# Performance work log

Measured on AMD Instinct MI355X. Metric: run time of the kernel, lower is better.

Reference implementation:

```python
import jax, jax.numpy as jnp
import numpy as np

BN_EPS = 1e-5
D_SLICE = 3  # forward slices last (neighbor) dim to :3 (d=3 in original code)


def _conv_bn_relu(x, W, b, gamma, beta):
    # x: (B, Cin, N, K) ; W: (Cout, Cin) ; 1x1 Conv2d + eval-mode BatchNorm(mean=0, var=1) + ReLU
    y = jnp.einsum('oi,bink->bonk', W, x) + b[:, None, None]
    y = gamma[:, None, None] * (y / jnp.sqrt(1.0 + BN_EPS)) + beta[:, None, None]
    return jax.nn.relu(y)


def setup_inputs() -> dict:
    key = jax.random.key(0)
    ks = jax.random.split(key, 16)
    B, N, K, C = 4, 32768, 16, 64
    mlp = [128, 64, 64]
    cin = C + 4  # feature + relation (diff_xyz 3 + distance 1)
    inp = {
        'src_xyz': jax.random.normal(ks[0], (B, 3, N, K), dtype=jnp.float32),
        'tgt_xyz': jax.random.normal(ks[1], (B, 3, N), dtype=jnp.float32),
        'feature': jax.random.normal(ks[2], (B, C, N, K), dtype=jnp.float32),
    }
    c_prev = cin
    for i, c_out in enumerate(mlp):
        scale = 1.0 / np.sqrt(c_prev)
        inp[f'W{i+1}'] = jax.random.uniform(ks[3 + 4 * i], (c_out, c_prev), minval=-scale, maxval=scale, dtype=jnp.float32)
        inp[f'b{i+1}'] = jax.random.uniform(ks[4 + 4 * i], (c_out,), minval=-scale, maxval=scale, dtype=jnp.float32)
        inp[f'g{i+1}'] = jnp.ones((c_out,), dtype=jnp.float32)
        inp[f'be{i+1}'] = jnp.zeros((c_out,), dtype=jnp.float32)
        c_prev = c_out
    return inp


def reference(src_xyz, tgt_xyz, feature, W1, b1, g1, be1, W2, b2, g2, be2, W3, b3, g3, be3):
    # relation feature on first D_SLICE neighbors (faithful to feature[:,:,:,:d], d=3)
    diff_xyz = src_xyz[:, :, :, :D_SLICE] - tgt_xyz[:, :, :, None]        # (B,3,N,3)
    distance = jnp.sum(diff_xyz ** 2, axis=1, keepdims=True)             # (B,1,N,3)
    x = jnp.concatenate([feature[:, :, :, :D_SLICE], diff_xyz, distance], axis=1)  # (B,C+4,N,3)
    x = _conv_bn_relu(x, W1, b1, g1, be1)
    x = _conv_bn_relu(x, W2, b2, g2, be2)
    x = _conv_bn_relu(x, W3, b3, g3, be3)
    return jnp.sum(x, axis=3)  # reduction='sum' over neighbor dim -> (B,64,N)
```

## Files before the change

kernel.cpp:

```cpp
#include <hip/hip_runtime.h>
#include <math.h>

typedef __attribute__((ext_vector_type(8))) short short8;
typedef __attribute__((ext_vector_type(4))) short short4v;
typedef __attribute__((ext_vector_type(4))) float f32x4;
typedef __attribute__((ext_vector_type(16))) float f32x16;

constexpr int BLOCK = 512;
constexpr int B_ = 4, C_ = 64, N_ = 32768, K_ = 16;
constexpr int P_ = 32;
constexpr int NCOL = 96;
constexpr int NF32 = 36, NF16 = 8;
constexpr int BIAS_OFF = (NF32 + NF16) * 1024;

constexpr int H2STR = 776;

__device__ __forceinline__ void bf16split(float f, short &hi, short &lo) {
    unsigned u  = __builtin_bit_cast(unsigned, f);
    unsigned hb = (u + 0x7FFFu + ((u >> 16) & 1u)) & 0xFFFF0000u;
    float hf    = __builtin_bit_cast(float, hb);
    hi = (short)(hb >> 16);
    float lf    = f - hf;
    unsigned ul = __builtin_bit_cast(unsigned, lf);
    lo = (short)((ul + 0x7FFFu + ((ul >> 16) & 1u)) >> 16);
}

__device__ __forceinline__ f32x4 mm16(short8 a, short8 b, f32x4 c) {
    return __builtin_amdgcn_mfma_f32_16x16x32_bf16(a, b, c, 0, 0, 0);
}
__device__ __forceinline__ f32x16 mm32(short8 a, short8 b, f32x16 c) {
    return __builtin_amdgcn_mfma_f32_32x32x16_bf16(a, b, c, 0, 0, 0);
}

__global__ void prep_wfrags(const float* __restrict__ W1, const float* __restrict__ g1,
                            const float* __restrict__ b1, const float* __restrict__ be1,
                            const float* __restrict__ W2, const float* __restrict__ g2,
                            const float* __restrict__ b2, const float* __restrict__ be2,
                            const float* __restrict__ W3, const float* __restrict__ g3,
                            const float* __restrict__ b3, const float* __restrict__ be3,
                            unsigned short* __restrict__ wf)
{
    const int gid = blockIdx.x * 256 + threadIdx.x;
    const float RS = 1.0f / sqrtf(1.0f + 1e-5f);
    const int NT = (NF32 + NF16) * 64;
    if (gid < NT) {
        const int f = gid >> 6, l = gid & 63;
        const float *W, *g; int CI, co, kb;
        if (f < 20)      { W = W1; g = g1; CI = 68;
                           co = (f / 5) * 32 + (l & 31);        kb = (f % 5) * 16 + (l >> 5) * 8; }
        else if (f < 36) { W = W2; g = g2; CI = 128;
                           co = ((f - 20) / 8) * 32 + (l & 31); kb = ((f - 20) % 8) * 16 + (l >> 5) * 8; }
        else             { W = W3; g = g3; CI = 64;
                           co = ((f - 36) / 2) * 16 + (l & 15); kb = ((f - 36) % 2) * 32 + (l >> 4) * 8; }
        const float gs = g[co] * RS;
        short8 h8, l8;
#pragma unroll
        for (int j = 0; j < 8; ++j) {
            const int k = kb + j;
            const float w = (k < CI) ? W[(size_t)co * CI + k] * gs : 0.0f;
            short hi, lo; bf16split(w, hi, lo);
            h8[j] = hi; l8[j] = lo;
        }
        *reinterpret_cast<short8*>(wf + (size_t)f * 1024 + l * 8)       = h8;
        *reinterpret_cast<short8*>(wf + (size_t)f * 1024 + 512 + l * 8) = l8;
    } else if (gid < NT + 256) {
        const int c = gid - NT;
        float* fb = reinterpret_cast<float*>(wf + BIAS_OFF);
        if (c < 128)      fb[c] = b1[c] * (g1[c] * RS) + be1[c];
        else if (c < 192) { const int q = c - 128; fb[c] = b2[q] * (g2[q] * RS) + be2[q]; }
        else              { const int q = c - 192; fb[c] = b3[q] * (g3[q] * RS) + be3[q]; }
    }
}

__device__ __forceinline__ void ldfrag(const unsigned short* __restrict__ wf,
                                       int f, int l, short8 &h, short8 &lo) {
    h  = *reinterpret_cast<const short8*>(wf + (size_t)f * 1024 + l * 8);
    lo = *reinterpret_cast<const short8*>(wf + (size_t)f * 1024 + 512 + l * 8);
}

__global__ __launch_bounds__(BLOCK, 4)
void mvp_mfma(const float* __restrict__ src, const float* __restrict__ tgt,
              const float* __restrict__ feat,
              const unsigned short* __restrict__ wf,
              float* __restrict__ out)
{
    __shared__ __align__(16) unsigned short xh_hi[10*768], xh_lo[10*768];
    __shared__ __align__(16) unsigned short h1_hi[16*768], h1_lo[16*768];

    const int tid = threadIdx.x;
    const int w   = tid >> 6;
    const int l   = tid & 63;
    const int b   = blockIdx.x >> 10;
    const int n0  = (blockIdx.x & 1023) << 5;

    if (tid < 96) {
        const int o = (9*96 + tid) * 8;
        const short8 z = {0,0,0,0,0,0,0,0};
        *reinterpret_cast<short8*>(&xh_hi[o]) = z;
        *reinterpret_cast<short8*>(&xh_lo[o]) = z;
    } else if (tid < 192) {
        const int o = (8*96 + (tid - 96)) * 8 + 4;
        const short4v z = {0,0,0,0};
        *reinterpret_cast<short4v*>(&xh_hi[o]) = z;
        *reinterpret_cast<short4v*>(&xh_lo[o]) = z;
    }
#pragma unroll
    for (int it = 0; it < 4; ++it) {
        const int idx = tid + it * BLOCK;
        const int c = idx >> 5, p = idx & 31;
        const float4 f = *reinterpret_cast<const float4*>(
            feat + ((size_t)(b*C_ + c) * N_ + (n0 + p)) * K_);
        const float v[3] = {f.x, f.y, f.z};
#pragma unroll
        for (int k = 0; k < 3; ++k) {
            short hi, lo; bf16split(v[k], hi, lo);
            const int off = ((c >> 3)*96 + k*32 + p)*8 + (c & 7);
            xh_hi[off] = (unsigned short)hi; xh_lo[off] = (unsigned short)lo;
        }
    }
    if (tid < 96) {
        const int p = tid & 31, k = tid >> 5;
        const int n = n0 + p;
        float d[4];
        d[0] = src[((size_t)(b*3+0)*N_ + n)*K_ + k] - tgt[(size_t)(b*3+0)*N_ + n];
        d[1] = src[((size_t)(b*3+1)*N_ + n)*K_ + k] - tgt[(size_t)(b*3+1)*N_ + n];
        d[2] = src[((size_t)(b*3+2)*N_ + n)*K_ + k] - tgt[(size_t)(b*3+2)*N_ + n];
        d[3] = d[0]*d[0] + d[1]*d[1] + d[2]*d[2];
        const int base = (8*96 + k*32 + p)*8;
#pragma unroll
        for (int j = 0; j < 4; ++j) {
            short hi, lo; bf16split(d[j], hi, lo);
            xh_hi[base + j] = (unsigned short)hi;
            xh_lo[base + j] = (unsigned short)lo;
        }
    }
    __syncthreads();

    const int hi32 = l >> 5, c32 = l & 31;
    const int lq = l >> 4, lr = l & 15, rq = lq << 2;
    const float* fb = reinterpret_cast<const float*>(wf + BIAS_OFF);

    {
        const int npass = (w < 4) ? 2 : 1;
        for (int pass = 0; pass < npass; ++pass) {
            const int t = pass ? (8 + w) : w;
            const int m = t / 3, n = t % 3;
            short8 ah[5], al[5];
#pragma unroll
            for (int ks = 0; ks < 5; ++ks) ldfrag(wf, m*5 + ks, l, ah[ks], al[ks]);
            f32x16 acc;
#pragma unroll
            for (int j = 0; j < 16; ++j) acc[j] = 0.0f;
#pragma unroll
            for (int ks = 0; ks < 5; ++ks) {
                const int so = ((ks*2 + hi32)*96 + n*32 + c32)*8;
                const short8 bh = *reinterpret_cast<const short8*>(&xh_hi[so]);
                const short8 bl = *reinterpret_cast<const short8*>(&xh_lo[so]);
                acc = mm32(ah[ks], bh, acc);
                acc = mm32(al[ks], bh, acc);
                acc = mm32(ah[ks], bl, acc);
            }
#pragma unroll
            for (int g = 0; g < 4; ++g) {
                const int co0 = m*32 + 8*g + 4*hi32;
                const float4 bb = *reinterpret_cast<const float4*>(fb + co0);
                const float bbv[4] = {bb.x, bb.y, bb.z, bb.w};
                short4v h4, l4;
#pragma unroll
                for (int r = 0; r < 4; ++r) {
                    const float v = fmaxf(acc[g*4 + r] + bbv[r], 0.0f);
                    short hh, ll; bf16split(v, hh, ll);
                    h4[r] = hh; l4[r] = ll;
                }
                const int so = ((m*4 + g)*96 + n*32 + c32)*8 + 4*hi32;
                *reinterpret_cast<short4v*>(&h1_hi[so]) = h4;
                *reinterpret_cast<short4v*>(&h1_lo[so]) = l4;
            }
        }
    }
    __syncthreads();

    if (w < 6) {
        const int m = w / 3, n = w % 3;
        short8 ah[8], al[8];
#pragma unroll
        for (int ks = 0; ks < 8; ++ks) ldfrag(wf, 20 + m*8 + ks, l, ah[ks], al[ks]);
        f32x16 acc;
#pragma unroll
        for (int j = 0; j < 16; ++j) acc[j] = 0.0f;
#pragma unroll
        for (int ks = 0; ks < 8; ++ks) {
            const int so = ((ks*2 + hi32)*96 + n*32 + c32)*8;
            const short8 bh = *reinterpret_cast<const short8*>(&h1_hi[so]);
            const short8 bl = *reinterpret_cast<const short8*>(&h1_lo[so]);
            acc = mm32(ah[ks], bh, acc);
            acc = mm32(al[ks], bh, acc);
            acc = mm32(ah[ks], bl, acc);
        }
#pragma unroll
        for (int g = 0; g < 4; ++g) {
            const int co0 = m*32 + 8*g + 4*hi32;
            const float4 bb = *reinterpret_cast<const float4*>(fb + 128 + co0);
            const float bbv[4] = {bb.x, bb.y, bb.z, bb.w};
            short4v h4, l4;
#pragma unroll
            for (int r = 0; r < 4; ++r) {
                const float v = fmaxf(acc[g*4 + r] + bbv[r], 0.0f);
                short hh, ll; bf16split(v, hh, ll);
                h4[r] = hh; l4[r] = ll;
            }
            const int so = (m*4 + g)*H2STR + (n*32 + c32)*8 + 4*hi32;
            *reinterpret_cast<short4v*>(&xh_hi[so]) = h4;
            *reinterpret_cast<short4v*>(&xh_lo[so]) = l4;
        }
    }
    __syncthreads();

    {
        const int m = w >> 1, hh = w & 1;
        short8 ah[2], al[2];
#pragma unroll
        for (int ks = 0; ks < 2; ++ks) ldfrag(wf, 36 + m*2 + ks, l, ah[ks], al[ks]);
        f32x4 acc3[3] = {f32x4{0,0,0,0}, f32x4{0,0,0,0}, f32x4{0,0,0,0}};
#pragma unroll
        for (int ks = 0; ks < 2; ++ks) {
#pragma unroll
            for (int t = 0; t < 3; ++t) {
                const int so = (ks*4 + lq)*H2STR + (t*32 + hh*16 + lr)*8;
                const short8 bh = *reinterpret_cast<const short8*>(&xh_hi[so]);
                const short8 bl = *reinterpret_cast<const short8*>(&xh_lo[so]);
                acc3[t] = mm16(ah[ks], bh, acc3[t]);
                acc3[t] = mm16(al[ks], bh, acc3[t]);
                acc3[t] = mm16(ah[ks], bl, acc3[t]);
            }
        }
        const int co0 = m*16 + rq;
        const float4 bb = *reinterpret_cast<const float4*>(fb + 192 + co0);
        const float bbv[4] = {bb.x, bb.y, bb.z, bb.w};
#pragma unroll
        for (int r = 0; r < 4; ++r) {
            float s = 0.0f;
#pragma unroll
            for (int t = 0; t < 3; ++t) s += fmaxf(acc3[t][r] + bbv[r], 0.0f);
            out[(size_t)(b*64 + co0 + r) * N_ + n0 + hh*16 + lr] = s;
        }
    }
}

extern "C" void kernel_launch(void* const* d_in, const int* in_sizes, int n_in,
                              void* d_out, int out_size, void* d_ws, size_t ws_size,
                              hipStream_t stream) {
    const float* src  = (const float*)d_in[0];
    const float* tgt  = (const float*)d_in[1];
    const float* feat = (const float*)d_in[2];
    const float* W1 = (const float*)d_in[3];
    const float* b1 = (const float*)d_in[4];
    const float* g1 = (const float*)d_in[5];
    const float* be1= (const float*)d_in[6];
    const float* W2 = (const float*)d_in[7];
    const float* b2 = (const float*)d_in[8];
    const float* g2 = (const float*)d_in[9];
    const float* be2= (const float*)d_in[10];
    const float* W3 = (const float*)d_in[11];
    const float* b3 = (const float*)d_in[12];
    const float* g3 = (const float*)d_in[13];
    const float* be3= (const float*)d_in[14];
    float* out = (float*)d_out;
    unsigned short* wfrag = (unsigned short*)d_ws;

    prep_wfrags<<<12, 256, 0, stream>>>(W1, g1, b1, be1, W2, g2, b2, be2,
                                        W3, g3, b3, be3, wfrag);

    const int grid = B_ * (N_ / P_);
    mvp_mfma<<<grid, BLOCK, 0, stream>>>(src, tgt, feat, wfrag, out);
}
```

Measured before the change: 159.6 us.

## Use fp16 single activations with split fp16 weights for layers two and three

Layers two and three now store hidden activations as one fp16 value instead of a bf16 hi/lo pair, and use fp16 MFMA with the weight split into fp16 hi plus residual. That drops one MFMA per step and halves LDS traffic for those activations. The smaller LDS footprint (shared buffer reuse, single h1 array) lets launch bounds rise to six blocks per CU, and layer one skips the padded k-slab for the upper half-lanes. fp16 activations risk range overflow or lost precision versus the previous three-term bf16 scheme.

```diff
diff --git a/kernel.cpp b/kernel.cpp
--- a/kernel.cpp
+++ b/kernel.cpp
@@ -5,14 +5,16 @@
 typedef __attribute__((ext_vector_type(4))) short short4v;
 typedef __attribute__((ext_vector_type(4))) float f32x4;
 typedef __attribute__((ext_vector_type(16))) float f32x16;
+typedef _Float16 half8 __attribute__((ext_vector_type(8)));
 
 constexpr int BLOCK = 512;
 constexpr int B_ = 4, C_ = 64, N_ = 32768, K_ = 16;
 constexpr int P_ = 32;
-constexpr int NCOL = 96;
-constexpr int NF32 = 36, NF16 = 8;
-constexpr int BIAS_OFF = (NF32 + NF16) * 1024;
-
+constexpr int NFRAG = 44;
+constexpr int BIAS_OFF = NFRAG * 1024;
+
+constexpr int ZOFF = 9 * 768;
+constexpr int XSZ  = 6920;
 constexpr int H2STR = 776;
 
 __device__ __forceinline__ void bf16split(float f, short &hi, short &lo) {
@@ -25,11 +27,18 @@
     lo = (short)((ul + 0x7FFFu + ((ul >> 16) & 1u)) >> 16);
 }
 
-__device__ __forceinline__ f32x4 mm16(short8 a, short8 b, f32x4 c) {
-    return __builtin_amdgcn_mfma_f32_16x16x32_bf16(a, b, c, 0, 0, 0);
-}
-__device__ __forceinline__ f32x16 mm32(short8 a, short8 b, f32x16 c) {
+__device__ __forceinline__ short f16bits(float v) {
+    return (short)__builtin_bit_cast(unsigned short, (_Float16)v);
+}
+
+__device__ __forceinline__ f32x16 mm32b(short8 a, short8 b, f32x16 c) {
     return __builtin_amdgcn_mfma_f32_32x32x16_bf16(a, b, c, 0, 0, 0);
+}
+__device__ __forceinline__ f32x16 mm32h(half8 a, half8 b, f32x16 c) {
+    return __builtin_amdgcn_mfma_f32_32x32x16_f16(a, b, c, 0, 0, 0);
+}
+__device__ __forceinline__ f32x4 mm16h(half8 a, half8 b, f32x4 c) {
+    return __builtin_amdgcn_mfma_f32_16x16x32_f16(a, b, c, 0, 0, 0);
 }
 
 __global__ void prep_wfrags(const float* __restrict__ W1, const float* __restrict__ g1,
@@ -42,7 +51,7 @@
 {
     const int gid = blockIdx.x * 256 + threadIdx.x;
     const float RS = 1.0f / sqrtf(1.0f + 1e-5f);
-    const int NT = (NF32 + NF16) * 64;
+    const int NT = NFRAG * 64;
     if (gid < NT) {
         const int f = gid >> 6, l = gid & 63;
         const float *W, *g; int CI, co, kb;
@@ -58,7 +67,14 @@
         for (int j = 0; j < 8; ++j) {
             const int k = kb + j;
             const float w = (k < CI) ? W[(size_t)co * CI + k] * gs : 0.0f;
-            short hi, lo; bf16split(w, hi, lo);
+            short hi, lo;
+            if (f < 20) {
+                bf16split(w, hi, lo);
+            } else {
+                _Float16 hf = (_Float16)w;
+                hi = (short)__builtin_bit_cast(unsigned short, hf);
+                lo = f16bits(w - (float)hf);
+            }
             h8[j] = hi; l8[j] = lo;
         }
         *reinterpret_cast<short8*>(wf + (size_t)f * 1024 + l * 8)       = h8;
@@ -78,14 +94,14 @@
     lo = *reinterpret_cast<const short8*>(wf + (size_t)f * 1024 + 512 + l * 8);
 }
 
-__global__ __launch_bounds__(BLOCK, 4)
+__global__ __launch_bounds__(BLOCK, 6)
 void mvp_mfma(const float* __restrict__ src, const float* __restrict__ tgt,
               const float* __restrict__ feat,
               const unsigned short* __restrict__ wf,
               float* __restrict__ out)
 {
-    __shared__ __align__(16) unsigned short xh_hi[10*768], xh_lo[10*768];
-    __shared__ __align__(16) unsigned short h1_hi[16*768], h1_lo[16*768];
+    __shared__ __align__(16) unsigned short xa_hi[XSZ], xa_lo[XSZ];
+    __shared__ __align__(16) unsigned short h1f[16*768];
 
     const int tid = threadIdx.x;
     const int w   = tid >> 6;
@@ -93,16 +109,16 @@
     const int b   = blockIdx.x >> 10;
     const int n0  = (blockIdx.x & 1023) << 5;
 
+    unsigned short* h2f = xa_hi;
+
     if (tid < 96) {
-        const int o = (9*96 + tid) * 8;
+        const int o = (8*96 + tid) * 8 + 4;
+        const short4v z = {0,0,0,0};
+        *reinterpret_cast<short4v*>(&xa_hi[o]) = z;
+        *reinterpret_cast<short4v*>(&xa_lo[o]) = z;
+    } else if (tid < 98) {
         const short8 z = {0,0,0,0,0,0,0,0};
-        *reinterpret_cast<short8*>(&xh_hi[o]) = z;
-        *reinterpret_cast<short8*>(&xh_lo[o]) = z;
-    } else if (tid < 192) {
-        const int o = (8*96 + (tid - 96)) * 8 + 4;
-        const short4v z = {0,0,0,0};
-        *reinterpret_cast<short4v*>(&xh_hi[o]) = z;
-        *reinterpret_cast<short4v*>(&xh_lo[o]) = z;
+        *reinterpret_cast<short8*>((tid == 96 ? xa_hi : xa_lo) + ZOFF) = z;
     }
 #pragma unroll
     for (int it = 0; it < 4; ++it) {
@@ -115,7 +131,7 @@
         for (int k = 0; k < 3; ++k) {
             short hi, lo; bf16split(v[k], hi, lo);
             const int off = ((c >> 3)*96 + k*32 + p)*8 + (c & 7);
-            xh_hi[off] = (unsigned short)hi; xh_lo[off] = (unsigned short)lo;
+            xa_hi[off] = (unsigned short)hi; xa_lo[off] = (unsigned short)lo;
         }
     }
     if (tid < 96) {
@@ -130,8 +146,8 @@
 #pragma unroll
         for (int j = 0; j < 4; ++j) {
             short hi, lo; bf16split(d[j], hi, lo);
-            xh_hi[base + j] = (unsigned short)hi;
-            xh_lo[base + j] = (unsigned short)lo;
+            xa_hi[base + j] = (unsigned short)hi;
+            xa_lo[base + j] = (unsigned short)lo;
         }
     }
     __syncthreads();
@@ -145,6 +161,7 @@
         for (int pass = 0; pass < npass; ++pass) {
             const int t = pass ? (8 + w) : w;
             const int m = t / 3, n = t % 3;
+            const int col = n*32 + c32;
             short8 ah[5], al[5];
 #pragma unroll
             for (int ks = 0; ks < 5; ++ks) ldfrag(wf, m*5 + ks, l, ah[ks], al[ks]);
@@ -152,29 +169,33 @@
 #pragma unroll
             for (int j = 0; j < 16; ++j) acc[j] = 0.0f;
 #pragma unroll
-            for (int ks = 0; ks < 5; ++ks) {
-                const int so = ((ks*2 + hi32)*96 + n*32 + c32)*8;
-                const short8 bh = *reinterpret_cast<const short8*>(&xh_hi[so]);
-                const short8 bl = *reinterpret_cast<const short8*>(&xh_lo[so]);
-                acc = mm32(ah[ks], bh, acc);
-                acc = mm32(al[ks], bh, acc);
-                acc = mm32(ah[ks], bl, acc);
+            for (int ks = 0; ks < 4; ++ks) {
+                const int so = ((ks*2 + hi32)*96 + col)*8;
+                const short8 bh = *reinterpret_cast<const short8*>(&xa_hi[so]);
+                const short8 bl = *reinterpret_cast<const short8*>(&xa_lo[so]);
+                acc = mm32b(ah[ks], bh, acc);
+                acc = mm32b(al[ks], bh, acc);
+                acc = mm32b(ah[ks], bl, acc);
+            }
+            {
+                const int so = hi32 ? ZOFF : (8*96 + col)*8;
+                const short8 bh = *reinterpret_cast<const short8*>(&xa_hi[so]);
+                const short8 bl = *reinterpret_cast<const short8*>(&xa_lo[so]);
+                acc = mm32b(ah[4], bh, acc);
+                acc = mm32b(al[4], bh, acc);
+                acc = mm32b(ah[4], bl, acc);
             }
 #pragma unroll
             for (int g = 0; g < 4; ++g) {
                 const int co0 = m*32 + 8*g + 4*hi32;
                 const float4 bb = *reinterpret_cast<const float4*>(fb + co0);
                 const float bbv[4] = {bb.x, bb.y, bb.z, bb.w};
-                short4v h4, l4;
-#pragma unroll
-                for (int r = 0; r < 4; ++r) {
-                    const float v = fmaxf(acc[g*4 + r] + bbv[r], 0.0f);
-                    short hh, ll; bf16split(v, hh, ll);
-                    h4[r] = hh; l4[r] = ll;
-                }
-                const int so = ((m*4 + g)*96 + n*32 + c32)*8 + 4*hi32;
-                *reinterpret_cast<short4v*>(&h1_hi[so]) = h4;
-                *reinterpret_cast<short4v*>(&h1_lo[so]) = l4;
+                short4v h4;
+#pragma unroll
+                for (int r = 0; r < 4; ++r)
+                    h4[r] = f16bits(fmaxf(acc[g*4 + r] + bbv[r], 0.0f));
+                const int so = ((m*4 + g)*96 + col)*8 + 4*hi32;
+                *reinterpret_cast<short4v*>(&h1f[so]) = h4;
             }
         }
     }
@@ -182,36 +203,31 @@
 
     if (w < 6) {
         const int m = w / 3, n = w % 3;
-        short8 ah[8], al[8];
-#pragma unroll
-        for (int ks = 0; ks < 8; ++ks) ldfrag(wf, 20 + m*8 + ks, l, ah[ks], al[ks]);
+        const int col = n*32 + c32;
         f32x16 acc;
 #pragma unroll
         for (int j = 0; j < 16; ++j) acc[j] = 0.0f;
 #pragma unroll
         for (int ks = 0; ks < 8; ++ks) {
-            const int so = ((ks*2 + hi32)*96 + n*32 + c32)*8;
-            const short8 bh = *reinterpret_cast<const short8*>(&h1_hi[so]);
-            const short8 bl = *reinterpret_cast<const short8*>(&h1_lo[so]);
-            acc = mm32(ah[ks], bh, acc);
-            acc = mm32(al[ks], bh, acc);
-            acc = mm32(ah[ks], bl, acc);
+            short8 ahs, als;
+            ldfrag(wf, 20 + m*8 + ks, l, ahs, als);
+            const int so = ((ks*2 + hi32)*96 + col)*8;
+            const half8 bh = __builtin_bit_cast(half8,
+                *reinterpret_cast<const short8*>(&h1f[so]));
+            acc = mm32h(__builtin_bit_cast(half8, ahs), bh, acc);
+            acc = mm32h(__builtin_bit_cast(half8, als), bh, acc);
         }
 #pragma unroll
         for (int g = 0; g < 4; ++g) {
             const int co0 = m*32 + 8*g + 4*hi32;
             const float4 bb = *reinterpret_cast<const float4*>(fb + 128 + co0);
             const float bbv[4] = {bb.x, bb.y, bb.z, bb.w};
-            short4v h4, l4;
-#pragma unroll
-            for (int r = 0; r < 4; ++r) {
-                const float v = fmaxf(acc[g*4 + r] + bbv[r], 0.0f);
-                short hh, ll; bf16split(v, hh, ll);
-                h4[r] = hh; l4[r] = ll;
-            }
-            const int so = (m*4 + g)*H2STR + (n*32 + c32)*8 + 4*hi32;
-            *reinterpret_cast<short4v*>(&xh_hi[so]) = h4;
-            *reinterpret_cast<short4v*>(&xh_lo[so]) = l4;
+            short4v h4;
+#pragma unroll
+            for (int r = 0; r < 4; ++r)
+                h4[r] = f16bits(fmaxf(acc[g*4 + r] + bbv[r], 0.0f));
+            const int so = (m*4 + g)*H2STR + col*8 + 4*hi32;
+            *reinterpret_cast<short4v*>(&h2f[so]) = h4;
         }
     }
     __syncthreads();
@@ -227,11 +243,10 @@
 #pragma unroll
             for (int t = 0; t < 3; ++t) {
                 const int so = (ks*4 + lq)*H2STR + (t*32 + hh*16 + lr)*8;
-                const short8 bh = *reinterpret_cast<const short8*>(&xh_hi[so]);
-                const short8 bl = *reinterpret_cast<const short8*>(&xh_lo[so]);
-                acc3[t] = mm16(ah[ks], bh, acc3[t]);
-                acc3[t] = mm16(al[ks], bh, acc3[t]);
-                acc3[t] = mm16(ah[ks], bl, acc3[t]);
+                const half8 bh = __builtin_bit_cast(half8,
+                    *reinterpret_cast<const short8*>(&h2f[so]));
+                acc3[t] = mm16h(__builtin_bit_cast(half8, ah[ks]), bh, acc3[t]);
+                acc3[t] = mm16h(__builtin_bit_cast(half8, al[ks]), bh, acc3[t]);
             }
         }
         const int co0 = m*16 + rq;
```

After: 143.3 us. 10.2% less time.
